# Optimization experiments

Measured on AMD Instinct MI355X. Metric: run time of the kernel, lower is better.

The kernel has to match this reference:

```python
import jax, jax.numpy as jnp
import numpy as np

E = 1024   # embed_dim
H = 16     # num_heads
R = 256    # rank
HD = E // H
B, S = 2, 2048


def setup_inputs() -> dict:
    key = jax.random.key(0)
    ks = jax.random.split(key, 20)
    sc = 0.02
    d = {
        'query': jax.random.normal(ks[0], (B, S, E), jnp.float32),
        'key':   jax.random.normal(ks[1], (B, S, E), jnp.float32),
        'value': jax.random.normal(ks[2], (B, S, E), jnp.float32),
    }
    names = ['q', 'k', 'v', 'o']
    i = 3
    for n in names:
        d[f'W{n}_lo'] = jax.random.normal(ks[i], (E, R), jnp.float32) * sc; i += 1
        d[f'b{n}_lo'] = jnp.zeros((R,), jnp.float32)
        d[f'W{n}_hi'] = jax.random.normal(ks[i], (R, E), jnp.float32) * sc; i += 1
        d[f'b{n}_hi'] = jnp.zeros((E,), jnp.float32)
    return d


def _lowrank(x, W_lo, b_lo, W_hi, b_hi):
    # Linear(E->R) then Linear(R->E)
    return (x @ W_lo + b_lo) @ W_hi + b_hi


def reference(query, key, value,
              Wq_lo, bq_lo, Wq_hi, bq_hi,
              Wk_lo, bk_lo, Wk_hi, bk_hi,
              Wv_lo, bv_lo, Wv_hi, bv_hi,
              Wo_lo, bo_lo, Wo_hi, bo_hi):
    b, s, _ = query.shape
    q = _lowrank(query, Wq_lo, bq_lo, Wq_hi, bq_hi)
    k = _lowrank(key,   Wk_lo, bk_lo, Wk_hi, bk_hi)
    v = _lowrank(value, Wv_lo, bv_lo, Wv_hi, bv_hi)
    # (B, S, E) -> (B, H, S, HD)
    q = q.reshape(b, s, H, HD).transpose(0, 2, 1, 3)
    k = k.reshape(b, s, H, HD).transpose(0, 2, 1, 3)
    v = v.reshape(b, s, H, HD).transpose(0, 2, 1, 3)
    scores = jnp.einsum('bhqd,bhkd->bhqk', q, k) / jnp.sqrt(jnp.float32(HD))
    attn = jax.nn.softmax(scores, axis=-1)  # dropout p=0.0 -> identity
    out = jnp.einsum('bhqk,bhkd->bhqd', attn, v)
    out = out.transpose(0, 2, 1, 3).reshape(b, s, E)
    return _lowrank(out, Wo_lo, bo_lo, Wo_hi, bo_hi)
```

## Files before the change

### kernel.cpp

```cpp
#include <hip/hip_runtime.h>

namespace {

constexpr int kE  = 1024;
constexpr int kH  = 16;
constexpr int kR  = 256;
constexpr int kHD = 64;
constexpr int kB  = 2;
constexpr int kS  = 2048;
constexpr int kM  = kB * kS;

typedef float  floatx4 __attribute__((ext_vector_type(4)));
typedef short  short8  __attribute__((ext_vector_type(8)));
typedef short  short4  __attribute__((ext_vector_type(4)));

__device__ inline short f2bf(float f) {
  union { float f; unsigned u; } x{f};
  unsigned r = x.u + 0x7FFF + ((x.u >> 16) & 1);
  return (short)(r >> 16);
}

__device__ inline void async_copy16(const void* g, void* l) {
  __builtin_amdgcn_global_load_lds(
      (const __attribute__((address_space(1))) unsigned int*)g,
      (__attribute__((address_space(3))) unsigned int*)l,
      16, 0, 0);
}

#if defined(__HIP_DEVICE_COMPILE__)
  #if __has_builtin(__builtin_amdgcn_mfma_f32_16x16x16bf16_1k)
    #define MFMA16(a, b, c) __builtin_amdgcn_mfma_f32_16x16x16bf16_1k(a, b, c, 0, 0, 0)
  #elif __has_builtin(__builtin_amdgcn_mfma_f32_16x16x16_bf16)
    #define MFMA16(a, b, c) __builtin_amdgcn_mfma_f32_16x16x16_bf16(a, b, c, 0, 0, 0)
  #else
    #error "no 16x16x16 bf16 MFMA builtin on device"
  #endif
#else
  #define MFMA16(a, b, c) (c)
#endif

struct PrepArgs { const float* src[8]; short* dst[8]; };

__global__ __launch_bounds__(256) void prep_weights(PrepArgs pa) {
  const int id = blockIdx.y;
  const bool lo = (id & 1) == 0;
  const int K = lo ? 1024 : 256;
  const int N = lo ? 256 : 1024;
  const int tiles_k = K >> 6;
  const int k0 = (blockIdx.x % tiles_k) * 64;
  const int n0 = (blockIdx.x / tiles_k) * 64;
  const float* src = pa.src[id];
  short* dst = pa.dst[id];

  __shared__ float tile[64][68];
  const int t  = threadIdx.x;
  const int c4 = (t & 15) * 4;
  const int r  = t >> 4;

#pragma unroll
  for (int i = 0; i < 4; ++i) {
    const int rk = r + i * 16;
    *(float4*)&tile[rk][c4] = *(const float4*)&src[(size_t)(k0 + rk) * N + n0 + c4];
  }
  __syncthreads();
#pragma unroll
  for (int i = 0; i < 4; ++i) {
    const int rn = r + i * 16;
    short4 o = { f2bf(tile[c4 + 0][rn]), f2bf(tile[c4 + 1][rn]),
                 f2bf(tile[c4 + 2][rn]), f2bf(tile[c4 + 3][rn]) };
    *(short4*)&dst[(size_t)(n0 + rn) * K + k0 + c4] = o;
  }
}

__global__ __launch_bounds__(256) void convert_in(
    const float* q, const float* k, const float* v,
    short* xq, short* xk, short* xv)
{
  const float* srcs[3] = {q, k, v};
  short* dsts[3] = {xq, xk, xv};
  const float* s = srcs[blockIdx.y];
  short* d = dsts[blockIdx.y];
  const size_t i = ((size_t)blockIdx.x * 256 + threadIdx.x) * 8;
  float4 a = *(const float4*)(s + i);
  float4 b = *(const float4*)(s + i + 4);
  short8 o = { f2bf(a.x), f2bf(a.y), f2bf(a.z), f2bf(a.w),
               f2bf(b.x), f2bf(b.y), f2bf(b.z), f2bf(b.w) };
  *(short8*)(d + i) = o;
}

struct GemmArgs {
  const short* A[3]; const short* Bt[3]; const float* bias[3];
  void* C[3]; float scale[3];
};

template <int N, int K, int BM, int BN, int MODE>
__global__ __launch_bounds__(256) void gemm_bf16(GemmArgs args) {
  constexpr int TILES_N = N / BN;
  constexpr int WTM = BM / 2, WTN = BN / 2;
  constexpr int FI = WTM / 16, FJ = WTN / 16;
  constexpr int AROUNDS = (BM * 64) / 4096;
  constexpr int BROUNDS = (BN * 64) / 4096;

  const int z = blockIdx.y;
  const int row0 = (blockIdx.x / TILES_N) * BM;
  const int col0 = (blockIdx.x % TILES_N) * BN;
  const short* A  = args.A[z];
  const short* Bt = args.Bt[z];
  const float* bias = args.bias[z];
  const float scale = args.scale[z];

  __shared__ short As[BM * 32];
  __shared__ short Bs[BN * 32];

  const int t    = threadIdx.x;
  const int wave = t >> 6;
  const int lane = t & 63;
  const int lq   = lane & 15;
  const int quad = lane >> 4;
  const int wm0  = (wave >> 1) * WTM;
  const int wn0  = (wave & 1) * WTN;

  const int srow = t >> 2;
  const int scol = (t & 3) * 8;

  floatx4 acc[FI][FJ] = {};

  for (int kk = 0; kk < K; kk += 32) {
#pragma unroll
    for (int r = 0; r < AROUNDS; ++r)
      async_copy16(A + (size_t)(row0 + r * 64 + srow) * K + kk + scol,
                   (char*)As + r * 4096 + wave * 1024);
#pragma unroll
    for (int r = 0; r < BROUNDS; ++r)
      async_copy16(Bt + (size_t)(col0 + r * 64 + srow) * K + kk + scol,
                   (char*)Bs + r * 4096 + wave * 1024);
    __syncthreads();

    short8 af[FI], bf[FJ];
#pragma unroll
    for (int i = 0; i < FI; ++i)
      af[i] = *(const short8*)((const char*)As + ((wm0 + i * 16 + lq) * 64 + quad * 16));
#pragma unroll
    for (int j = 0; j < FJ; ++j)
      bf[j] = *(const short8*)((const char*)Bs + ((wn0 + j * 16 + lq) * 64 + quad * 16));
#pragma unroll
    for (int i = 0; i < FI; ++i)
#pragma unroll
      for (int j = 0; j < FJ; ++j)
        acc[i][j] = __builtin_amdgcn_mfma_f32_16x16x32_bf16(af[i], bf[j], acc[i][j], 0, 0, 0);
    __syncthreads();
  }

#pragma unroll
  for (int i = 0; i < FI; ++i) {
    const int rbase = row0 + wm0 + i * 16 + quad * 4;
#pragma unroll
    for (int j = 0; j < FJ; ++j) {
      const int col = col0 + wn0 + j * 16 + lq;
      const float bj = bias[col];
      if (MODE == 2) {
        float* C = (float*)args.C[z];
#pragma unroll
        for (int r = 0; r < 4; ++r)
          C[(size_t)(rbase + r) * N + col] = (acc[i][j][r] + bj) * scale;
      } else if (MODE == 1) {
        short* C = (short*)args.C[z];
        const int h = col >> 6, d = col & 63;
        const int b = rbase >> 11, s = rbase & 2047;
        if (z == 2) {
          short4 o = { f2bf(acc[i][j][0] + bj), f2bf(acc[i][j][1] + bj),
                       f2bf(acc[i][j][2] + bj), f2bf(acc[i][j][3] + bj) };
          *(short4*)&C[((size_t)((b * 16 + h) * 64 + d)) * 2048 + s] = o;
        } else {
#pragma unroll
          for (int r = 0; r < 4; ++r)
            C[((size_t)((b * 16 + h) * 2048 + s + r)) * 64 + d] =
                f2bf((acc[i][j][r] + bj) * scale);
        }
      } else {
        short* C = (short*)args.C[z];
#pragma unroll
        for (int r = 0; r < 4; ++r)
          C[(size_t)(rbase + r) * N + col] = f2bf((acc[i][j][r] + bj) * scale);
      }
    }
  }
}

__global__ __launch_bounds__(256) void attn_mfma(
    const short* __restrict__ Qp, const short* __restrict__ Kp,
    const short* __restrict__ Vtp, short* __restrict__ O)
{
  __shared__ short Ks[64][72];
  __shared__ short Vs[64][72];

  const int t    = threadIdx.x;
  const int wave = t >> 6;
  const int lane = t & 63;
  const int lq   = lane & 15;
  const int quad = lane >> 4;

  const int q0 = blockIdx.x * 64;
  const int bh = blockIdx.y;
  const int b  = bh >> 4;
  const int h  = bh & 15;

  const short* qrow = Qp + ((size_t)bh * kS + q0 + wave * 16 + lq) * 64;
  short8 qf0 = *(const short8*)(qrow + quad * 8);
  short8 qf1 = *(const short8*)(qrow + 32 + quad * 8);

  const short* Kbase = Kp  + (size_t)bh * kS * 64;
  const short* Vbase = Vtp + (size_t)bh * 64 * kS;

  const int srow = wave * 16 + (lane >> 3);
  const int scol = (lane & 7) * 8;

  floatx4 Oacc[4] = {};
  float m = -1e30f;
  float l = 0.f;

  short8 gk0 = *(const short8*)(Kbase + (size_t)(srow) * 64 + scol);
  short8 gk1 = *(const short8*)(Kbase + (size_t)(srow + 8) * 64 + scol);
  short8 gv0 = *(const short8*)(Vbase + (size_t)srow * kS + scol);
  short8 gv1 = *(const short8*)(Vbase + (size_t)(srow + 8) * kS + scol);

  for (int kc = 0; kc < kS; kc += 64) {
    __syncthreads();
    *(short8*)&Ks[srow][scol]     = gk0;
    *(short8*)&Ks[srow + 8][scol] = gk1;
    *(short8*)&Vs[srow][scol]     = gv0;
    *(short8*)&Vs[srow + 8][scol] = gv1;
    __syncthreads();

    if (kc + 64 < kS) {
      gk0 = *(const short8*)(Kbase + (size_t)(kc + 64 + srow) * 64 + scol);
      gk1 = *(const short8*)(Kbase + (size_t)(kc + 64 + srow + 8) * 64 + scol);
      gv0 = *(const short8*)(Vbase + (size_t)srow * kS + kc + 64 + scol);
      gv1 = *(const short8*)(Vbase + (size_t)(srow + 8) * kS + kc + 64 + scol);
    }

    floatx4 Sc[4];
#pragma unroll
    for (int tt = 0; tt < 4; ++tt) {
      short8 a0 = *(const short8*)&Ks[tt * 16 + lq][quad * 8];
      short8 a1 = *(const short8*)&Ks[tt * 16 + lq][32 + quad * 8];
      floatx4 c = {};
      c = __builtin_amdgcn_mfma_f32_16x16x32_bf16(a0, qf0, c, 0, 0, 0);
      c = __builtin_amdgcn_mfma_f32_16x16x32_bf16(a1, qf1, c, 0, 0, 0);
      Sc[tt] = c;
    }

    float mc = -1e30f;
#pragma unroll
    for (int tt = 0; tt < 4; ++tt)
#pragma unroll
      for (int r = 0; r < 4; ++r) mc = fmaxf(mc, Sc[tt][r]);
    mc = fmaxf(mc, __shfl_xor(mc, 16, 64));
    mc = fmaxf(mc, __shfl_xor(mc, 32, 64));
    const float mn = fmaxf(m, mc);
    const float alpha = __expf(m - mn);
    m = mn;

    float ls = 0.f;
    short4 pf[4];
#pragma unroll
    for (int tt = 0; tt < 4; ++tt) {
      float p0 = __expf(Sc[tt][0] - m);
      float p1 = __expf(Sc[tt][1] - m);
      float p2 = __expf(Sc[tt][2] - m);
      float p3 = __expf(Sc[tt][3] - m);
      ls += (p0 + p1) + (p2 + p3);
      pf[tt] = short4{ f2bf(p0), f2bf(p1), f2bf(p2), f2bf(p3) };
    }
    l = l * alpha + ls;
#pragma unroll
    for (int dt = 0; dt < 4; ++dt)
#pragma unroll
      for (int r = 0; r < 4; ++r) Oacc[dt][r] *= alpha;

#pragma unroll
    for (int dt = 0; dt < 4; ++dt) {
#pragma unroll
      for (int tt = 0; tt < 4; ++tt) {
        short4 vf = *(const short4*)&Vs[dt * 16 + lq][tt * 16 + quad * 4];
        Oacc[dt] = MFMA16(vf, pf[tt], Oacc[dt]);
      }
    }
  }

  l += __shfl_xor(l, 16, 64);
  l += __shfl_xor(l, 32, 64);
  const float inv = 1.f / l;

  short* orow = O + ((size_t)(b * kS + q0 + wave * 16 + lq)) * kE + h * kHD;
#pragma unroll
  for (int dt = 0; dt < 4; ++dt) {
    short4 o = { f2bf(Oacc[dt][0] * inv), f2bf(Oacc[dt][1] * inv),
                 f2bf(Oacc[dt][2] * inv), f2bf(Oacc[dt][3] * inv) };
    *(short4*)&orow[dt * 16 + quad * 4] = o;
  }
}

}

extern "C" void kernel_launch(void* const* d_in, const int* in_sizes, int n_in,
                              void* d_out, int out_size, void* d_ws, size_t ws_size,
                              hipStream_t stream) {
  short* ws = (short*)d_ws;
  short* Xq  = ws;
  short* Xk  = Xq  + (size_t)kM * kE;
  short* Xv  = Xk  + (size_t)kM * kE;
  short* Tq  = Xv  + (size_t)kM * kE;
  short* Tk  = Tq  + (size_t)kM * kR;
  short* Tv  = Tk  + (size_t)kM * kR;
  short* Qh  = Tv  + (size_t)kM * kR;
  short* Kh  = Qh  + (size_t)kM * kE;
  short* Vth = Kh  + (size_t)kM * kE;
  short* Ab  = Vth + (size_t)kM * kE;
  short* To  = Ab  + (size_t)kM * kE;
  short* Wt  = To  + (size_t)kM * kR;

  short* WtArr[8];
  for (int i = 0; i < 8; ++i) WtArr[i] = Wt + (size_t)i * (kE * kR);

  PrepArgs pa;
  const int widx[8] = {3, 5, 7, 9, 11, 13, 15, 17};
  for (int i = 0; i < 8; ++i) { pa.src[i] = (const float*)d_in[widx[i]]; pa.dst[i] = WtArr[i]; }
  prep_weights<<<dim3(64, 8), dim3(256), 0, stream>>>(pa);

  convert_in<<<dim3((kM * kE) / (256 * 8), 3), dim3(256), 0, stream>>>(
      (const float*)d_in[0], (const float*)d_in[1], (const float*)d_in[2], Xq, Xk, Xv);

  {
    GemmArgs ga;
    ga.A[0] = Xq; ga.A[1] = Xk; ga.A[2] = Xv;
    ga.Bt[0] = WtArr[0]; ga.Bt[1] = WtArr[2]; ga.Bt[2] = WtArr[4];
    ga.bias[0] = (const float*)d_in[4]; ga.bias[1] = (const float*)d_in[8]; ga.bias[2] = (const float*)d_in[12];
    ga.C[0] = Tq; ga.C[1] = Tk; ga.C[2] = Tv;
    ga.scale[0] = ga.scale[1] = ga.scale[2] = 1.f;
    gemm_bf16<kR, kE, 64, 64, 0><<<dim3((kM / 64) * (kR / 64), 3), dim3(256), 0, stream>>>(ga);
  }

  {
    GemmArgs ga;
    ga.A[0] = Tq; ga.A[1] = Tk; ga.A[2] = Tv;
    ga.Bt[0] = WtArr[1]; ga.Bt[1] = WtArr[3]; ga.Bt[2] = WtArr[5];
    ga.bias[0] = (const float*)d_in[6]; ga.bias[1] = (const float*)d_in[10]; ga.bias[2] = (const float*)d_in[14];
    ga.C[0] = Qh; ga.C[1] = Kh; ga.C[2] = Vth;
    ga.scale[0] = 0.125f; ga.scale[1] = 1.f; ga.scale[2] = 1.f;
    gemm_bf16<kE, kR, 128, 128, 1><<<dim3((kM / 128) * (kE / 128), 3), dim3(256), 0, stream>>>(ga);
  }

  attn_mfma<<<dim3(kS / 64, kB * kH), dim3(256), 0, stream>>>(Qh, Kh, Vth, Ab);

  {
    GemmArgs ga;
    ga.A[0] = Ab; ga.Bt[0] = WtArr[6];
    ga.bias[0] = (const float*)d_in[16];
    ga.C[0] = To; ga.scale[0] = 1.f;
    gemm_bf16<kR, kE, 64, 64, 0><<<dim3((kM / 64) * (kR / 64), 1), dim3(256), 0, stream>>>(ga);
  }
  {
    GemmArgs ga;
    ga.A[0] = To; ga.Bt[0] = WtArr[7];
    ga.bias[0] = (const float*)d_in[18];
    ga.C[0] = d_out; ga.scale[0] = 1.f;
    gemm_bf16<kE, kR, 128, 128, 2><<<dim3((kM / 128) * (kE / 128), 1), dim3(256), 0, stream>>>(ga);
  }
}
```

Measured before the change: 261.9 us.

## Fuse input fp32 conversion into GEMM, double-buffer GEMM/attention tiles, use exp2 softmax

```diff
diff --git a/kernel.cpp b/kernel.cpp
--- a/kernel.cpp
+++ b/kernel.cpp
@@ -18,6 +18,23 @@
   union { float f; unsigned u; } x{f};
   unsigned r = x.u + 0x7FFF + ((x.u >> 16) & 1);
   return (short)(r >> 16);
+}
+
+__device__ inline unsigned pack2bf(float a, float b) {
+#if defined(__HIP_DEVICE_COMPILE__)
+  unsigned ua = __float_as_uint(a) + 0x8000u;
+  unsigned ub = __float_as_uint(b) + 0x8000u;
+  return __builtin_amdgcn_perm(ub, ua, 0x07060302u);
+#else
+  (void)a; (void)b; return 0;
+#endif
+}
+
+__device__ inline short4 pack4bf(float p0, float p1, float p2, float p3) {
+  union { unsigned u[2]; short4 s; } r;
+  r.u[0] = pack2bf(p0, p1);
+  r.u[1] = pack2bf(p2, p3);
+  return r.s;
 }
 
 __device__ inline void async_copy16(const void* g, void* l) {
@@ -72,45 +89,31 @@
   }
 }
 
-__global__ __launch_bounds__(256) void convert_in(
-    const float* q, const float* k, const float* v,
-    short* xq, short* xk, short* xv)
-{
-  const float* srcs[3] = {q, k, v};
-  short* dsts[3] = {xq, xk, xv};
-  const float* s = srcs[blockIdx.y];
-  short* d = dsts[blockIdx.y];
-  const size_t i = ((size_t)blockIdx.x * 256 + threadIdx.x) * 8;
-  float4 a = *(const float4*)(s + i);
-  float4 b = *(const float4*)(s + i + 4);
-  short8 o = { f2bf(a.x), f2bf(a.y), f2bf(a.z), f2bf(a.w),
-               f2bf(b.x), f2bf(b.y), f2bf(b.z), f2bf(b.w) };
-  *(short8*)(d + i) = o;
-}
-
 struct GemmArgs {
-  const short* A[3]; const short* Bt[3]; const float* bias[3];
+  const void* A[3]; const short* Bt[3]; const float* bias[3];
   void* C[3]; float scale[3];
 };
 
-template <int N, int K, int BM, int BN, int MODE>
-__global__ __launch_bounds__(256) void gemm_bf16(GemmArgs args) {
+template <int N, int K, int BM, int BN, int MODE, bool AF32>
+__global__ __launch_bounds__(256) void gemm_k(GemmArgs args) {
+  static_assert(!AF32 || BM == 64, "AF32 staging assumes BM=64");
   constexpr int TILES_N = N / BN;
   constexpr int WTM = BM / 2, WTN = BN / 2;
   constexpr int FI = WTM / 16, FJ = WTN / 16;
-  constexpr int AROUNDS = (BM * 64) / 4096;
-  constexpr int BROUNDS = (BN * 64) / 4096;
+  constexpr int BR = (BN * 128) / 4096;
+  constexpr int AR = (BM * 128) / 4096;
 
   const int z = blockIdx.y;
   const int row0 = (blockIdx.x / TILES_N) * BM;
   const int col0 = (blockIdx.x % TILES_N) * BN;
-  const short* A  = args.A[z];
   const short* Bt = args.Bt[z];
   const float* bias = args.bias[z];
   const float scale = args.scale[z];
-
-  __shared__ short As[BM * 32];
-  __shared__ short Bs[BN * 32];
+  const float* Af = (const float*)args.A[z];
+  const short* Ah = (const short*)args.A[z];
+
+  __shared__ short As[2][BM * 64];
+  __shared__ short Bs[2][BN * 64];
 
   const int t    = threadIdx.x;
   const int wave = t >> 6;
@@ -120,35 +123,63 @@
   const int wm0  = (wave >> 1) * WTM;
   const int wn0  = (wave & 1) * WTN;
 
-  const int srow = t >> 2;
-  const int scol = (t & 3) * 8;
+  auto stageB = [&](int buf, int kk) {
+#pragma unroll
+    for (int r = 0; r < BR; ++r)
+      async_copy16(Bt + (size_t)(col0 + r * 32 + wave * 8 + (lane >> 3)) * K + kk + (lane & 7) * 8,
+                   (char*)Bs[buf] + r * 4096 + wave * 1024);
+  };
+  auto stageA = [&](int buf, int kk) {
+    if constexpr (AF32) {
+#pragma unroll
+      for (int r = 0; r < 2; ++r) {
+        const int i = r * 256 + t;
+        const int row = i >> 3, blk = i & 7;
+        const float* src = Af + (size_t)(row0 + row) * K + kk + blk * 8;
+        float4 x = *(const float4*)src;
+        float4 y = *(const float4*)(src + 4);
+        unsigned* dst = (unsigned*)&As[buf][row * 64 + (blk ^ (row & 7)) * 8];
+        dst[0] = pack2bf(x.x, x.y);
+        dst[1] = pack2bf(x.z, x.w);
+        dst[2] = pack2bf(y.x, y.y);
+        dst[3] = pack2bf(y.z, y.w);
+      }
+    } else {
+#pragma unroll
+      for (int r = 0; r < AR; ++r)
+        async_copy16(Ah + (size_t)(row0 + r * 32 + wave * 8 + (lane >> 3)) * K + kk + (lane & 7) * 8,
+                     (char*)As[buf] + r * 4096 + wave * 1024);
+    }
+  };
 
   floatx4 acc[FI][FJ] = {};
-
-  for (int kk = 0; kk < K; kk += 32) {
-#pragma unroll
-    for (int r = 0; r < AROUNDS; ++r)
-      async_copy16(A + (size_t)(row0 + r * 64 + srow) * K + kk + scol,
-                   (char*)As + r * 4096 + wave * 1024);
-#pragma unroll
-    for (int r = 0; r < BROUNDS; ++r)
-      async_copy16(Bt + (size_t)(col0 + r * 64 + srow) * K + kk + scol,
-                   (char*)Bs + r * 4096 + wave * 1024);
+  stageB(0, 0);
+  stageA(0, 0);
+  int buf = 0;
+
+  for (int kk = 0; kk < K; kk += 64) {
     __syncthreads();
-
-    short8 af[FI], bf[FJ];
-#pragma unroll
-    for (int i = 0; i < FI; ++i)
-      af[i] = *(const short8*)((const char*)As + ((wm0 + i * 16 + lq) * 64 + quad * 16));
-#pragma unroll
-    for (int j = 0; j < FJ; ++j)
-      bf[j] = *(const short8*)((const char*)Bs + ((wn0 + j * 16 + lq) * 64 + quad * 16));
-#pragma unroll
-    for (int i = 0; i < FI; ++i)
+    if (kk + 64 < K) { stageB(buf ^ 1, kk + 64); stageA(buf ^ 1, kk + 64); }
+
+#pragma unroll
+    for (int ks = 0; ks < 2; ++ks) {
+      short8 af[FI], bf[FJ];
+#pragma unroll
+      for (int i = 0; i < FI; ++i) {
+        int blk = 4 * ks + quad;
+        if constexpr (AF32) blk ^= (lq & 7);
+        af[i] = *(const short8*)&As[buf][(wm0 + i * 16 + lq) * 64 + blk * 8];
+      }
 #pragma unroll
       for (int j = 0; j < FJ; ++j)
-        acc[i][j] = __builtin_amdgcn_mfma_f32_16x16x32_bf16(af[i], bf[j], acc[i][j], 0, 0, 0);
-    __syncthreads();
+        bf[j] = *(const short8*)&Bs[buf][(wn0 + j * 16 + lq) * 64 + ks * 32 + quad * 8];
+#pragma unroll
+      for (int i = 0; i < FI; ++i)
+#pragma unroll
+        for (int j = 0; j < FJ; ++j)
+          acc[i][j] = __builtin_amdgcn_mfma_f32_16x16x32_bf16(af[i], bf[j], acc[i][j], 0, 0, 0);
+    }
+    buf ^= 1;
   }
 
 #pragma unroll
@@ -168,8 +199,8 @@
         const int h = col >> 6, d = col & 63;
         const int b = rbase >> 11, s = rbase & 2047;
         if (z == 2) {
-          short4 o = { f2bf(acc[i][j][0] + bj), f2bf(acc[i][j][1] + bj),
-                       f2bf(acc[i][j][2] + bj), f2bf(acc[i][j][3] + bj) };
+          short4 o = pack4bf(acc[i][j][0] + bj, acc[i][j][1] + bj,
+                             acc[i][j][2] + bj, acc[i][j][3] + bj);
           *(short4*)&C[((size_t)((b * 16 + h) * 64 + d)) * 2048 + s] = o;
         } else {
 #pragma unroll
@@ -191,8 +222,8 @@
     const short* __restrict__ Qp, const short* __restrict__ Kp,
     const short* __restrict__ Vtp, short* __restrict__ O)
 {
-  __shared__ short Ks[64][72];
-  __shared__ short Vs[64][72];
+  __shared__ short Ks[2][64 * 64];
+  __shared__ short Vs[2][64 * 64];
 
   const int t    = threadIdx.x;
   const int wave = t >> 6;
@@ -212,38 +243,43 @@
   const short* Kbase = Kp  + (size_t)bh * kS * 64;
   const short* Vbase = Vtp + (size_t)bh * 64 * kS;
 
-  const int srow = wave * 16 + (lane >> 3);
-  const int scol = (lane & 7) * 8;
+  const int srow  = wave * 16 + (lane >> 3);
+  const int sblk  = lane & 7;
+  const int swr   = srow * 64 + (sblk ^ (srow & 7)) * 8;
+  const short* kst = Kbase + (size_t)srow * 64 + sblk * 8;
+  const short* vst = Vbase + (size_t)srow * kS + sblk * 8;
 
   floatx4 Oacc[4] = {};
   float m = -1e30f;
   float l = 0.f;
 
-  short8 gk0 = *(const short8*)(Kbase + (size_t)(srow) * 64 + scol);
-  short8 gk1 = *(const short8*)(Kbase + (size_t)(srow + 8) * 64 + scol);
-  short8 gv0 = *(const short8*)(Vbase + (size_t)srow * kS + scol);
-  short8 gv1 = *(const short8*)(Vbase + (size_t)(srow + 8) * kS + scol);
-
+  short8 gk0 = *(const short8*)(kst);
+  short8 gk1 = *(const short8*)(kst + 8 * 64);
+  short8 gv0 = *(const short8*)(vst);
+  short8 gv1 = *(const short8*)(vst + 8 * kS);
+
+  int buf = 0;
   for (int kc = 0; kc < kS; kc += 64) {
+    *(short8*)&Ks[buf][swr]       = gk0;
+    *(short8*)&Ks[buf][swr + 512] = gk1;
+    *(short8*)&Vs[buf][swr]       = gv0;
+    *(short8*)&Vs[buf][swr + 512] = gv1;
     __syncthreads();
-    *(short8*)&Ks[srow][scol]     = gk0;
-    *(short8*)&Ks[srow + 8][scol] = gk1;
-    *(short8*)&Vs[srow][scol]     = gv0;
-    *(short8*)&Vs[srow + 8][scol] = gv1;
-    __syncthreads();
 
     if (kc + 64 < kS) {
-      gk0 = *(const short8*)(Kbase + (size_t)(kc + 64 + srow) * 64 + scol);
-      gk1 = *(const short8*)(Kbase + (size_t)(kc + 64 + srow + 8) * 64 + scol);
-      gv0 = *(const short8*)(Vbase + (size_t)srow * kS + kc + 64 + scol);
-      gv1 = *(const short8*)(Vbase + (size_t)(srow + 8) * kS + kc + 64 + scol);
+      gk0 = *(const short8*)(kst + (size_t)(kc + 64) * 64);
+      gk1 = *(const short8*)(kst + (size_t)(kc + 64) * 64 + 8 * 64);
+      gv0 = *(const short8*)(vst + kc + 64);
+      gv1 = *(const short8*)(vst + kc + 64 + 8 * kS);
     }
 
     floatx4 Sc[4];
 #pragma unroll
     for (int tt = 0; tt < 4; ++tt) {
-      short8 a0 = *(const short8*)&Ks[tt * 16 + lq][quad * 8];
-      short8 a1 = *(const short8*)&Ks[tt * 16 + lq][32 + quad * 8];
+      const int krow = (tt * 16 + lq) * 64;
+      const int xr   = lq & 7;
+      short8 a0 = *(const short8*)&Ks[buf][krow + (quad ^ xr) * 8];
+      short8 a1 = *(const short8*)&Ks[buf][krow + ((4 + quad) ^ xr) * 8];
       floatx4 c = {};
       c = __builtin_amdgcn_mfma_f32_16x16x32_bf16(a0, qf0, c, 0, 0, 0);
       c = __builtin_amdgcn_mfma_f32_16x16x32_bf16(a1, qf1, c, 0, 0, 0);
@@ -257,35 +293,41 @@
       for (int r = 0; r < 4; ++r) mc = fmaxf(mc, Sc[tt][r]);
     mc = fmaxf(mc, __shfl_xor(mc, 16, 64));
     mc = fmaxf(mc, __shfl_xor(mc, 32, 64));
-    const float mn = fmaxf(m, mc);
-    const float alpha = __expf(m - mn);
-    m = mn;
+    if (mc > m) {
+      const float alpha = exp2f(m - mc);
+      m = mc;
+      l *= alpha;
+#pragma unroll
+      for (int dt = 0; dt < 4; ++dt)
+#pragma unroll
+        for (int r = 0; r < 4; ++r) Oacc[dt][r] *= alpha;
+    }
 
     float ls = 0.f;
     short4 pf[4];
 #pragma unroll
     for (int tt = 0; tt < 4; ++tt) {
-      float p0 = __expf(Sc[tt][0] - m);
-      float p1 = __expf(Sc[tt][1] - m);
-      float p2 = __expf(Sc[tt][2] - m);
-      float p3 = __expf(Sc[tt][3] - m);
+      float p0 = exp2f(Sc[tt][0] - m);
+      float p1 = exp2f(Sc[tt][1] - m);
+      float p2 = exp2f(Sc[tt][2] - m);
+      float p3 = exp2f(Sc[tt][3] - m);
       ls += (p0 + p1) + (p2 + p3);
-      pf[tt] = short4{ f2bf(p0), f2bf(p1), f2bf(p2), f2bf(p3) };
-    }
-    l = l * alpha + ls;
-#pragma unroll
-    for (int dt = 0; dt < 4; ++dt)
-#pragma unroll
-      for (int r = 0; r < 4; ++r) Oacc[dt][r] *= alpha;
+      pf[tt] = pack4bf(p0, p1, p2, p3);
+    }
+    l += ls;
 
 #pragma unroll
     for (int dt = 0; dt < 4; ++dt) {
+      const int vrow = (dt * 16 + lq) * 64;
+      const int xr   = lq & 7;
 #pragma unroll
       for (int tt = 0; tt < 4; ++tt) {
-        short4 vf = *(const short4*)&Vs[dt * 16 + lq][tt * 16 + quad * 4];
+        short4 vf = *(const short4*)
+            &Vs[buf][vrow + ((2 * tt + (quad >> 1)) ^ xr) * 8 + (quad & 1) * 4];
         Oacc[dt] = MFMA16(vf, pf[tt], Oacc[dt]);
       }
     }
+    buf ^= 1;
   }
 
   l += __shfl_xor(l, 16, 64);
@@ -295,8 +337,8 @@
   short* orow = O + ((size_t)(b * kS + q0 + wave * 16 + lq)) * kE + h * kHD;
 #pragma unroll
   for (int dt = 0; dt < 4; ++dt) {
-    short4 o = { f2bf(Oacc[dt][0] * inv), f2bf(Oacc[dt][1] * inv),
-                 f2bf(Oacc[dt][2] * inv), f2bf(Oacc[dt][3] * inv) };
+    short4 o = pack4bf(Oacc[dt][0] * inv, Oacc[dt][1] * inv,
+                       Oacc[dt][2] * inv, Oacc[dt][3] * inv);
     *(short4*)&orow[dt * 16 + quad * 4] = o;
   }
 }
@@ -307,10 +349,7 @@
                               void* d_out, int out_size, void* d_ws, size_t ws_size,
                               hipStream_t stream) {
   short* ws = (short*)d_ws;
-  short* Xq  = ws;
-  short* Xk  = Xq  + (size_t)kM * kE;
-  short* Xv  = Xk  + (size_t)kM * kE;
-  short* Tq  = Xv  + (size_t)kM * kE;
+  short* Tq  = ws;
   short* Tk  = Tq  + (size_t)kM * kR;
   short* Tv  = Tk  + (size_t)kM * kR;
   short* Qh  = Tv  + (size_t)kM * kR;
@@ -323,22 +362,21 @@
   short* WtArr[8];
   for (int i = 0; i < 8; ++i) WtArr[i] = Wt + (size_t)i * (kE * kR);
 
+  constexpr float kQScale = 0.125f * 1.44269504088896341f;
+
   PrepArgs pa;
   const int widx[8] = {3, 5, 7, 9, 11, 13, 15, 17};
   for (int i = 0; i < 8; ++i) { pa.src[i] = (const float*)d_in[widx[i]]; pa.dst[i] = WtArr[i]; }
   prep_weights<<<dim3(64, 8), dim3(256), 0, stream>>>(pa);
 
-  convert_in<<<dim3((kM * kE) / (256 * 8), 3), dim3(256), 0, stream>>>(
-      (const float*)d_in[0], (const float*)d_in[1], (const float*)d_in[2], Xq, Xk, Xv);
-
   {
     GemmArgs ga;
-    ga.A[0] = Xq; ga.A[1] = Xk; ga.A[2] = Xv;
+    ga.A[0] = d_in[0]; ga.A[1] = d_in[1]; ga.A[2] = d_in[2];
     ga.Bt[0] = WtArr[0]; ga.Bt[1] = WtArr[2]; ga.Bt[2] = WtArr[4];
     ga.bias[0] = (const float*)d_in[4]; ga.bias[1] = (const float*)d_in[8]; ga.bias[2] = (const float*)d_in[12];
     ga.C[0] = Tq; ga.C[1] = Tk; ga.C[2] = Tv;
     ga.scale[0] = ga.scale[1] = ga.scale[2] = 1.f;
-    gemm_bf16<kR, kE, 64, 64, 0><<<dim3((kM / 64) * (kR / 64), 3), dim3(256), 0, stream>>>(ga);
+    gemm_k<kR, kE, 64, 64, 0, true><<<dim3((kM / 64) * (kR / 64), 3), dim3(256), 0, stream>>>(ga);
   }
 
   {
@@ -347,8 +385,8 @@
     ga.Bt[0] = WtArr[1]; ga.Bt[1] = WtArr[3]; ga.Bt[2] = WtArr[5];
     ga.bias[0] = (const float*)d_in[6]; ga.bias[1] = (const float*)d_in[10]; ga.bias[2] = (const float*)d_in[14];
     ga.C[0] = Qh; ga.C[1] = Kh; ga.C[2] = Vth;
-    ga.scale[0] = 0.125f; ga.scale[1] = 1.f; ga.scale[2] = 1.f;
-    gemm_bf16<kE, kR, 128, 128, 1><<<dim3((kM / 128) * (kE / 128), 3), dim3(256), 0, stream>>>(ga);
+    ga.scale[0] = kQScale; ga.scale[1] = 1.f; ga.scale[2] = 1.f;
+    gemm_k<kE, kR, 64, 128, 1, false><<<dim3((kM / 64) * (kE / 128), 3), dim3(256), 0, stream>>>(ga);
   }
 
   attn_mfma<<<dim3(kS / 64, kB * kH), dim3(256), 0, stream>>>(Qh, Kh, Vth, Ab);
@@ -358,13 +396,13 @@
     ga.A[0] = Ab; ga.Bt[0] = WtArr[6];
     ga.bias[0] = (const float*)d_in[16];
     ga.C[0] = To; ga.scale[0] = 1.f;
-    gemm_bf16<kR, kE, 64, 64, 0><<<dim3((kM / 64) * (kR / 64), 1), dim3(256), 0, stream>>>(ga);
+    gemm_k<kR, kE, 64, 64, 0, false><<<dim3((kM / 64) * (kR / 64), 1), dim3(256), 0, stream>>>(ga);
   }
   {
     GemmArgs ga;
     ga.A[0] = To; ga.Bt[0] = WtArr[7];
     ga.bias[0] = (const float*)d_in[18];
     ga.C[0] = d_out; ga.scale[0] = 1.f;
-    gemm_bf16<kE, kR, 128, 128, 2><<<dim3((kM / 128) * (kE / 128), 1), dim3(256), 0, stream>>>(ga);
-  }
-}
+    gemm_k<kE, kR, 64, 128, 2, false><<<dim3((kM / 64) * (kE / 128), 1), dim3(256), 0, stream>>>(ga);
+  }
+}
```

Result: slower. 287.9 us (+9.9%).
